# Optimization experiments

Measured on AMD Instinct MI355X. Metric: run time of the kernel, lower is better.

## Reference

```python
import jax, jax.numpy as jnp
import numpy as np

B, T1, T2, NFEAT, H = 8, 512, 1500, 1024, 16
DK = NFEAT // H


def setup_inputs() -> dict:
    key = jax.random.key(0)
    ks = jax.random.split(key, 8)
    s = 0.02
    return {
        "x": jax.random.normal(ks[0], (B, T1, NFEAT), dtype=jnp.float32),
        "memory": jax.random.normal(ks[1], (B, T2, NFEAT), dtype=jnp.float32),
        "memory_mask": jnp.ones((B, 1, T2), dtype=jnp.int32),
        "Wq": jax.random.normal(ks[2], (NFEAT, NFEAT), dtype=jnp.float32) * s,
        "bq": jnp.zeros((NFEAT,), dtype=jnp.float32),
        "Wkv": jax.random.normal(ks[3], (NFEAT, 2 * NFEAT), dtype=jnp.float32) * s,
        "bkv": jnp.zeros((2 * NFEAT,), dtype=jnp.float32),
        "Wout": jax.random.normal(ks[4], (NFEAT, NFEAT), dtype=jnp.float32) * s,
        "bout": jnp.zeros((NFEAT,), dtype=jnp.float32),
    }


def reference(x, memory, memory_mask, Wq, bq, Wkv, bkv, Wout, bout):
    b, t1, _ = x.shape
    t2 = memory.shape[1]
    # projections (W stored as (in, out))
    q = x @ Wq + bq                                   # (b, t1, n_feat)
    kv = memory @ Wkv + bkv                           # (b, t2, 2*n_feat)
    k, v = jnp.split(kv, 2, axis=-1)
    q_h = q.reshape(b, t1, H, DK).transpose(0, 2, 1, 3)   # (b,h,t1,dk)
    k_h = k.reshape(b, t2, H, DK).transpose(0, 2, 1, 3)   # (b,h,t2,dk)
    v_h = v.reshape(b, t2, H, DK).transpose(0, 2, 1, 3)   # (b,h,t2,dk)
    q_h = q_h * (DK ** -0.5)
    scores = jnp.einsum("bhqd,bhkd->bhqk", q_h, k_h)      # (b,h,t1,t2)
    mask0 = (memory_mask[:, None, :, :] == 0)             # (b,1,1 or t1,t2)
    scores = jnp.where(mask0, -jnp.inf, scores)
    attn = jax.nn.softmax(scores, axis=-1)
    attn = jnp.where(mask0, 0.0, attn)
    ctx = jnp.einsum("bhqk,bhkd->bhqd", attn, v_h)        # (b,h,t1,dk)
    ctx = ctx.transpose(0, 2, 1, 3).reshape(b, t1, H * DK)
    return ctx @ Wout + bout
```

## Files before the change

### kernel.cpp

```cpp
#include <hip/hip_runtime.h>
#include <cstdint>
#include <cstddef>

typedef __attribute__((ext_vector_type(8))) short short8;
typedef __attribute__((ext_vector_type(4))) float f32x4;

typedef __attribute__((address_space(3))) unsigned int lds_u32;
typedef const __attribute__((address_space(1))) unsigned int glb_u32;

__device__ __forceinline__ void gl_lds16(const void* g, void* l) {
  __builtin_amdgcn_global_load_lds((glb_u32*)g, (lds_u32*)l, 16, 0, 0);
}

__device__ __forceinline__ unsigned short bf16_rne(float f) {
  unsigned int u = __float_as_uint(f);
  u += 0x7FFFu + ((u >> 16) & 1u);
  return (unsigned short)(u >> 16);
}

__device__ __forceinline__ void cvt_body(const float* __restrict__ in,
                                         unsigned short* __restrict__ out,
                                         int i, int n8) {
  if (i >= n8) return;
  float4 a = reinterpret_cast<const float4*>(in)[2 * i];
  float4 b = reinterpret_cast<const float4*>(in)[2 * i + 1];
  short8 v;
  v[0] = (short)bf16_rne(a.x); v[1] = (short)bf16_rne(a.y);
  v[2] = (short)bf16_rne(a.z); v[3] = (short)bf16_rne(a.w);
  v[4] = (short)bf16_rne(b.x); v[5] = (short)bf16_rne(b.y);
  v[6] = (short)bf16_rne(b.z); v[7] = (short)bf16_rne(b.w);
  reinterpret_cast<short8*>(out)[i] = v;
}

__global__ void __launch_bounds__(256) k_prep(const float* __restrict__ x,
                                              const float* __restrict__ mem,
                                              const float* __restrict__ Wq,
                                              const float* __restrict__ Wkv,
                                              const float* __restrict__ Wout,
                                              unsigned short* __restrict__ xb,
                                              unsigned short* __restrict__ mb,
                                              unsigned short* __restrict__ wqT,
                                              unsigned short* __restrict__ wkvT,
                                              unsigned short* __restrict__ woutT,
                                              unsigned short* __restrict__ pk,
                                              unsigned short* __restrict__ pv) {
  __shared__ float t[64][65];
  const int bid = blockIdx.x, tid = threadIdx.x;
  if (bid < 2048) {
    cvt_body(x, xb, bid * 256 + tid, 524288);
  } else if (bid < 8048) {
    cvt_body(mem, mb, (bid - 2048) * 256 + tid, 1536000);
  } else if (bid < 9072) {
    const float* W; unsigned short* WT; int R = 1024, C; int bid2, bx, by;
    if (bid < 8304)      { W = Wq;   WT = wqT;   C = 1024; bid2 = bid - 8048; bx = bid2 & 15; by = bid2 >> 4; }
    else if (bid < 8816) { W = Wkv;  WT = wkvT;  C = 2048; bid2 = bid - 8304; bx = bid2 & 31; by = bid2 >> 5; }
    else                 { W = Wout; WT = woutT; C = 1024; bid2 = bid - 8816; bx = bid2 & 15; by = bid2 >> 4; }
    const int c0 = bx * 64, r0 = by * 64;
    const int lr = tid >> 6, lc = tid & 63;
#pragma unroll
    for (int i = 0; i < 16; ++i)
      t[i * 4 + lr][lc] = W[(size_t)(r0 + i * 4 + lr) * C + c0 + lc];
    __syncthreads();
#pragma unroll
    for (int i = 0; i < 16; ++i) {
      int ro = i * 4 + lr;
      WT[(size_t)(c0 + ro) * R + r0 + lc] = bf16_rne(t[lc][ro]);
    }
  } else {
    int i = (bid - 9072) * 256 + tid;
    if (i >= 128 * 36 * 64) return;
    int head = i / (36 * 64);
    int rem = i - head * (36 * 64);
    int t2 = rem / 64 + 1500;
    int dk = rem & 63;
    size_t ik = ((size_t)(head * 24 + 23) * 8 + (dk >> 3)) * 512 + (t2 & 63) * 8 + (dk & 7);
    size_t iv = ((size_t)(head * 24 + 23) * 8 + ((t2 >> 3) & 7)) * 512 + dk * 8 + (t2 & 7);
    pk[ik] = 0;
    pv[iv] = 0;
  }
}

template <int MODE>
__global__ void __launch_bounds__(256) k_gemm(const unsigned short* __restrict__ A,
                                              const unsigned short* __restrict__ BT,
                                              const float* __restrict__ bias,
                                              void* __restrict__ out1,
                                              void* __restrict__ out2,
                                              int M, int K) {
  __shared__ unsigned short As[128 * 64];
  __shared__ unsigned short Bs[128 * 64];
  const int tid = threadIdx.x;
  const int lane = tid & 63;
  const int wid = tid >> 6;
  const int grp = lane >> 4, lm = lane & 15;

  constexpr int NBY = (MODE == 1) ? 16 : 8;
  constexpr int NWG = (MODE == 1) ? 94 * 16 : 32 * 8;
  constexpr int CPX = NWG / 8;
  const int bid = blockIdx.x;
  const int logical = (bid & 7) * CPX + (bid >> 3);
  const int m0 = (logical / NBY) * 128, n0 = (logical % NBY) * 128;

  const int wm = (wid >> 1) * 64, wn = (wid & 1) * 64;
  const int srow = tid >> 3;
  const int sx = ((tid & 7) * 16) ^ ((srow & 7) << 4);

  f32x4 acc[4][4] = {};

  const int nkt = K >> 6;
  for (int kt = 0; kt < nkt; ++kt) {
    __syncthreads();
#pragma unroll
    for (int c = 0; c < 4; ++c) {
      int row = c * 32 + srow;
      int ra = m0 + row; if (ra > M - 1) ra = M - 1;
      gl_lds16(A + (size_t)ra * K + kt * 64 + (sx >> 1), As + c * 2048 + tid * 8);
      gl_lds16(BT + (size_t)(n0 + row) * K + kt * 64 + (sx >> 1), Bs + c * 2048 + tid * 8);
    }
    __syncthreads();

    short8 af[4][2], bfr[4][2];
#pragma unroll
    for (int m = 0; m < 4; ++m)
#pragma unroll
      for (int ks = 0; ks < 2; ++ks) {
        int row = wm + m * 16 + lm;
        int off = (ks * 64 + grp * 16) ^ ((row & 7) << 4);
        af[m][ks] = *reinterpret_cast<const short8*>(&As[row * 64 + (off >> 1)]);
      }
#pragma unroll
    for (int n = 0; n < 4; ++n)
#pragma unroll
      for (int ks = 0; ks < 2; ++ks) {
        int row = wn + n * 16 + lm;
        int off = (ks * 64 + grp * 16) ^ ((row & 7) << 4);
        bfr[n][ks] = *reinterpret_cast<const short8*>(&Bs[row * 64 + (off >> 1)]);
      }
#pragma unroll
    for (int m = 0; m < 4; ++m)
#pragma unroll
      for (int n = 0; n < 4; ++n)
#pragma unroll
        for (int ks = 0; ks < 2; ++ks)
          acc[m][n] = __builtin_amdgcn_mfma_f32_16x16x32_bf16(af[m][ks], bfr[n][ks],
                                                              acc[m][n], 0, 0, 0);
  }

#pragma unroll
  for (int m = 0; m < 4; ++m) {
    int rbase = m0 + wm + m * 16 + grp * 4;
#pragma unroll
    for (int n = 0; n < 4; ++n) {
      int cg = n0 + wn + n * 16 + lm;
      float bs = bias[cg];
#pragma unroll
      for (int r = 0; r < 4; ++r) {
        int row = rbase + r;
        float v = acc[m][n][r] + bs;
        if (MODE == 0) {
          v *= 0.180336884f;
          int b = row >> 9, t1 = row & 511, h = cg >> 6, dk = cg & 63;
          ((unsigned short*)out1)[(((size_t)b * 16 + h) * 512 + t1) * 64 + dk] = bf16_rne(v);
        } else if (MODE == 1) {
          if (row < M) {
            int b = row / 1500, t2 = row - b * 1500;
            if (cg < 1024) {
              int h = cg >> 6, dk = cg & 63;
              int head = b * 16 + h;
              size_t idx = ((size_t)(head * 24 + (t2 >> 6)) * 8 + (dk >> 3)) * 512 +
                           (t2 & 63) * 8 + (dk & 7);
              ((unsigned short*)out1)[idx] = bf16_rne(v);
            } else {
              int h = (cg - 1024) >> 6, dk = (cg - 1024) & 63;
              int head = b * 16 + h;
              size_t idx = ((size_t)(head * 24 + (t2 >> 6)) * 8 + ((t2 >> 3) & 7)) * 512 +
                           dk * 8 + (t2 & 7);
              ((unsigned short*)out2)[idx] = bf16_rne(v);
            }
          }
        } else {
          ((float*)out1)[(size_t)row * 1024 + cg] = v;
        }
      }
    }
  }
}

__global__ void __launch_bounds__(256) k_attn(const unsigned short* __restrict__ Q,
                                              const unsigned short* __restrict__ PK,
                                              const unsigned short* __restrict__ PV,
                                              const int* __restrict__ mask,
                                              float* __restrict__ po,
                                              float* __restrict__ dn) {
  __shared__ unsigned short Ps[4][16 * 64];
  const int tid = threadIdx.x, lane = tid & 63, wid = tid >> 6;
  const int grp = lane >> 4, lm = lane & 15;
  const int bid = blockIdx.x;
  const int logical = (bid & 7) * 256 + (bid >> 3);
  const int head = logical >> 4, qt = (logical >> 1) & 7, half = logical & 1;
  const int b = head >> 4, h = head & 15;
  const int kt0 = half * 12;

  const unsigned short* qbase = Q + ((size_t)head * 512 + qt * 64) * 64;
  const unsigned short* kf = PK + (size_t)head * 98304 + grp * 512 + lm * 8;
  const unsigned short* vf = PV + (size_t)head * 98304 + grp * 512 + lm * 8;
  const int* mrow = mask + b * 1500;

  short8 aq[2];
#pragma unroll
  for (int ks = 0; ks < 2; ++ks)
    aq[ks] = *reinterpret_cast<const short8*>(qbase + (wid * 16 + lm) * 64 + ks * 32 + grp * 8);

  unsigned long long mlo = 0ull;
#pragma unroll
  for (int i = 0; i < 48; ++i) {
    int col = (kt0 + (i >> 2)) * 64 + (i & 3) * 16 + lm;
    unsigned int ok = (col < 1500) ? (mrow[col] != 0 ? 1u : 0u) : 0u;
    mlo |= (unsigned long long)ok << i;
  }

  f32x4 O[4] = {};
  f32x4 O4 = {0.f, 0.f, 0.f, 0.f};
  const short8 onesb = {(short)0x3F80, (short)0x3F80, (short)0x3F80, (short)0x3F80,
                        (short)0x3F80, (short)0x3F80, (short)0x3F80, (short)0x3F80};

  short8 bk[4][2];
#pragma unroll
  for (int n = 0; n < 4; ++n)
#pragma unroll
    for (int ks = 0; ks < 2; ++ks)
      bk[n][ks] = *reinterpret_cast<const short8*>(kf + (size_t)kt0 * 4096 + ks * 2048 + n * 128);

  for (int kt = kt0; kt < kt0 + 12; ++kt) {
    short8 bv[4][2];
#pragma unroll
    for (int n2 = 0; n2 < 4; ++n2)
#pragma unroll
      for (int ks = 0; ks < 2; ++ks)
        bv[n2][ks] = *reinterpret_cast<const short8*>(vf + (size_t)kt * 4096 + ks * 2048 + n2 * 128);

    f32x4 s[4];
#pragma unroll
    for (int n = 0; n < 4; ++n) {
      s[n] = f32x4{0.f, 0.f, 0.f, 0.f};
#pragma unroll
      for (int ks = 0; ks < 2; ++ks)
        s[n] = __builtin_amdgcn_mfma_f32_16x16x32_bf16(aq[ks], bk[n][ks], s[n], 0, 0, 0);
    }

    if (kt < kt0 + 11) {
#pragma unroll
      for (int n = 0; n < 4; ++n)
#pragma unroll
        for (int ks = 0; ks < 2; ++ks)
          bk[n][ks] = *reinterpret_cast<const short8*>(
              kf + (size_t)(kt + 1) * 4096 + ks * 2048 + n * 128);
    }

    unsigned int nib = (unsigned int)mlo & 15u;
    mlo >>= 4;
    float mb4[4];
#pragma unroll
    for (int n = 0; n < 4; ++n) mb4[n] = (nib >> n) & 1u ? -8.0f : -3.0e38f;
#pragma unroll
    for (int n = 0; n < 4; ++n)
#pragma unroll
      for (int r = 0; r < 4; ++r) s[n][r] = exp2f(s[n][r] + mb4[n]);

#pragma unroll
    for (int n = 0; n < 4; ++n)
#pragma unroll
      for (int r = 0; r < 4; ++r) {
        int prow = grp * 4 + r;
        int pb = (n * 16 + lm) * 2;
        Ps[wid][prow * 64 + ((pb ^ ((prow & 7) << 4)) >> 1)] = bf16_rne(s[n][r]);
      }
    short8 pa[2];
#pragma unroll
    for (int ks = 0; ks < 2; ++ks) {
      int off = (ks * 64 + grp * 16) ^ ((lm & 7) << 4);
      pa[ks] = *reinterpret_cast<const short8*>(&Ps[wid][lm * 64 + (off >> 1)]);
    }

#pragma unroll
    for (int n2 = 0; n2 < 4; ++n2)
#pragma unroll
      for (int ks = 0; ks < 2; ++ks)
        O[n2] = __builtin_amdgcn_mfma_f32_16x16x32_bf16(pa[ks], bv[n2][ks], O[n2], 0, 0, 0);
#pragma unroll
    for (int ks = 0; ks < 2; ++ks)
      O4 = __builtin_amdgcn_mfma_f32_16x16x32_bf16(pa[ks], onesb, O4, 0, 0, 0);
  }

  float* orow = po + (size_t)half * 4194304 +
                ((size_t)(b * 512 + qt * 64 + wid * 16 + grp * 4)) * 1024 + h * 64;
#pragma unroll
  for (int r = 0; r < 4; ++r)
#pragma unroll
    for (int n2 = 0; n2 < 4; ++n2)
      orow[r * 1024 + n2 * 16 + lm] = O[n2][r];
  if (lm == 0) {
    int t1g = b * 512 + qt * 64 + wid * 16 + grp * 4;
#pragma unroll
    for (int r = 0; r < 4; ++r)
      dn[half * 65536 + (t1g + r) * 16 + h] = O4[r];
  }
}

__global__ void __launch_bounds__(256) k_comb(const float* __restrict__ po,
                                              const float* __restrict__ dn,
                                              unsigned short* __restrict__ ctx) {
  int idx = blockIdx.x * 256 + threadIdx.x;
  if (idx >= 524288) return;
  int row = idx >> 7, c8 = idx & 127;
  int col0 = c8 * 8, h = c8 >> 3;
  float d = dn[row * 16 + h] + dn[65536 + row * 16 + h];
  float inv = 1.0f / d;
  const float4* p0 = reinterpret_cast<const float4*>(po + (size_t)row * 1024 + col0);
  const float4* p1 = reinterpret_cast<const float4*>(po + 4194304 + (size_t)row * 1024 + col0);
  float4 a0 = p0[0], a1 = p0[1], b0 = p1[0], b1 = p1[1];
  short8 v;
  v[0] = (short)bf16_rne((a0.x + b0.x) * inv);
  v[1] = (short)bf16_rne((a0.y + b0.y) * inv);
  v[2] = (short)bf16_rne((a0.z + b0.z) * inv);
  v[3] = (short)bf16_rne((a0.w + b0.w) * inv);
  v[4] = (short)bf16_rne((a1.x + b1.x) * inv);
  v[5] = (short)bf16_rne((a1.y + b1.y) * inv);
  v[6] = (short)bf16_rne((a1.z + b1.z) * inv);
  v[7] = (short)bf16_rne((a1.w + b1.w) * inv);
  reinterpret_cast<short8*>(ctx)[idx] = v;
}

extern "C" void kernel_launch(void* const* d_in, const int* in_sizes, int n_in,
                              void* d_out, int out_size, void* d_ws, size_t ws_size,
                              hipStream_t stream) {
  const float* x = (const float*)d_in[0];
  const float* mem = (const float*)d_in[1];
  const int* mask = (const int*)d_in[2];
  const float* Wq = (const float*)d_in[3];
  const float* bq = (const float*)d_in[4];
  const float* Wkv = (const float*)d_in[5];
  const float* bkv = (const float*)d_in[6];
  const float* Wout = (const float*)d_in[7];
  const float* bout = (const float*)d_in[8];

  uint8_t* w = (uint8_t*)d_ws;
  unsigned short* xb    = (unsigned short*)(w);
  unsigned short* mb    = (unsigned short*)(w + 8388608);
  unsigned short* wqT   = (unsigned short*)(w + 32964608);
  unsigned short* wkvT  = (unsigned short*)(w + 35061760);
  unsigned short* woutT = (unsigned short*)(w + 39256064);
  unsigned short* qb    = (unsigned short*)(w + 41353216);
  unsigned short* kb    = (unsigned short*)(w + 49741824);
  unsigned short* vtb   = (unsigned short*)(w + 74907648);
  unsigned short* ctx   = (unsigned short*)(w + 100073472);
  float* po             = (float*)(w);
  float* dn             = (float*)(w + 33554432);

  k_prep<<<10224, 256, 0, stream>>>(x, mem, Wq, Wkv, Wout, xb, mb, wqT, wkvT, woutT, kb, vtb);
  k_gemm<0><<<256, 256, 0, stream>>>(xb, wqT, bq, qb, nullptr, 4096, 1024);
  k_gemm<1><<<1504, 256, 0, stream>>>(mb, wkvT, bkv, kb, vtb, 12000, 1024);
  k_attn<<<2048, 256, 0, stream>>>(qb, kb, vtb, mask, po, dn);
  k_comb<<<2048, 256, 0, stream>>>(po, dn, ctx);
  k_gemm<2><<<256, 256, 0, stream>>>(ctx, woutT, bout, d_out, nullptr, 4096, 1024);
}
```

Before: 222.3 us.

## Triple-buffer GEMM LDS loads and widen tiles to 128x256 with 512 threads

Reworks the projection GEMM kernel to use a three-stage LDS ring buffer, issuing global-to-LDS loads two k-tiles ahead and using vmcnt waits instead of a sync before and after every tile. Tiles grow to 128x256 with 8 waves per block, halving the grid sizes. The goal is to overlap memory loads with MFMA work and to reuse each A tile across more of N. In exchange, LDS per block rises to 144 KB, which caps occupancy at one block per CU, and the GEMM grids drop to 128 and 752 blocks, which may underfill the GPU. NKT is hardcoded to 16, which assumes K=1024.

```diff
diff --git a/kernel.cpp b/kernel.cpp
--- a/kernel.cpp
+++ b/kernel.cpp
@@ -81,43 +81,63 @@
 }
 
 template <int MODE>
-__global__ void __launch_bounds__(256) k_gemm(const unsigned short* __restrict__ A,
+__global__ void __launch_bounds__(512) k_gemm(const unsigned short* __restrict__ A,
                                               const unsigned short* __restrict__ BT,
                                               const float* __restrict__ bias,
                                               void* __restrict__ out1,
                                               void* __restrict__ out2,
                                               int M, int K) {
-  __shared__ unsigned short As[128 * 64];
-  __shared__ unsigned short Bs[128 * 64];
+  __shared__ unsigned short As[3][128 * 64];
+  __shared__ unsigned short Bs[3][256 * 64];
   const int tid = threadIdx.x;
   const int lane = tid & 63;
   const int wid = tid >> 6;
   const int grp = lane >> 4, lm = lane & 15;
 
-  constexpr int NBY = (MODE == 1) ? 16 : 8;
-  constexpr int NWG = (MODE == 1) ? 94 * 16 : 32 * 8;
+  constexpr int NBY = (MODE == 1) ? 8 : 4;
+  constexpr int NWG = (MODE == 1) ? 94 * 8 : 32 * 4;
   constexpr int CPX = NWG / 8;
   const int bid = blockIdx.x;
   const int logical = (bid & 7) * CPX + (bid >> 3);
-  const int m0 = (logical / NBY) * 128, n0 = (logical % NBY) * 128;
-
-  const int wm = (wid >> 1) * 64, wn = (wid & 1) * 64;
+  const int m0 = (logical / NBY) * 128, n0 = (logical % NBY) * 256;
+
+  const int wm = (wid >> 2) * 64, wn = (wid & 3) * 64;
   const int srow = tid >> 3;
-  const int sx = ((tid & 7) * 16) ^ ((srow & 7) << 4);
+  const int scolb = (tid & 7) * 16;
+
+  constexpr int NKT = 16;
+
+#define STAGE(kt, buf)                                                        \
+  {                                                                           \
+    _Pragma("unroll") for (int j = 0; j < 2; ++j) {                           \
+      int row = j * 64 + srow;                                                \
+      int sxb = scolb ^ ((row & 7) << 4);                                     \
+      int ra = m0 + row; if (ra > M - 1) ra = M - 1;                          \
+      gl_lds16(A + (size_t)ra * K + (kt) * 64 + (sxb >> 1),                   \
+               &As[buf][0] + j * 4096 + tid * 8);                             \
+    }                                                                         \
+    _Pragma("unroll") for (int j = 0; j < 4; ++j) {                           \
+      int row = j * 64 + srow;                                                \
+      int sxb = scolb ^ ((row & 7) << 4);                                     \
+      gl_lds16(BT + (size_t)(n0 + row) * K + (kt) * 64 + (sxb >> 1),          \
+               &Bs[buf][0] + j * 4096 + tid * 8);                             \
+    }                                                                         \
+  }
 
   f32x4 acc[4][4] = {};
 
-  const int nkt = K >> 6;
-  for (int kt = 0; kt < nkt; ++kt) {
-    __syncthreads();
-#pragma unroll
-    for (int c = 0; c < 4; ++c) {
-      int row = c * 32 + srow;
-      int ra = m0 + row; if (ra > M - 1) ra = M - 1;
-      gl_lds16(A + (size_t)ra * K + kt * 64 + (sx >> 1), As + c * 2048 + tid * 8);
-      gl_lds16(BT + (size_t)(n0 + row) * K + kt * 64 + (sx >> 1), Bs + c * 2048 + tid * 8);
-    }
-    __syncthreads();
+  STAGE(0, 0);
+  STAGE(1, 1);
+  asm volatile("s_waitcnt vmcnt(6)" ::: "memory");
+  __builtin_amdgcn_s_barrier();
+  __builtin_amdgcn_sched_barrier(0);
+
+  for (int t = 0; t < NKT; ++t) {
+    const int cb = t % 3;
+    if (t + 2 < NKT) {
+      const int nb = (t + 2) % 3;
+      if (nb == 0) STAGE(t + 2, 0) else if (nb == 1) STAGE(t + 2, 1) else STAGE(t + 2, 2);
+    }
 
     short8 af[4][2], bfr[4][2];
 #pragma unroll
@@ -126,7 +146,7 @@
       for (int ks = 0; ks < 2; ++ks) {
         int row = wm + m * 16 + lm;
         int off = (ks * 64 + grp * 16) ^ ((row & 7) << 4);
-        af[m][ks] = *reinterpret_cast<const short8*>(&As[row * 64 + (off >> 1)]);
+        af[m][ks] = *reinterpret_cast<const short8*>(&As[cb][row * 64 + (off >> 1)]);
       }
 #pragma unroll
     for (int n = 0; n < 4; ++n)
@@ -134,7 +154,7 @@
       for (int ks = 0; ks < 2; ++ks) {
         int row = wn + n * 16 + lm;
         int off = (ks * 64 + grp * 16) ^ ((row & 7) << 4);
-        bfr[n][ks] = *reinterpret_cast<const short8*>(&Bs[row * 64 + (off >> 1)]);
+        bfr[n][ks] = *reinterpret_cast<const short8*>(&Bs[cb][row * 64 + (off >> 1)]);
       }
 #pragma unroll
     for (int m = 0; m < 4; ++m)
@@ -144,7 +164,13 @@
         for (int ks = 0; ks < 2; ++ks)
           acc[m][n] = __builtin_amdgcn_mfma_f32_16x16x32_bf16(af[m][ks], bfr[n][ks],
                                                               acc[m][n], 0, 0, 0);
-  }
+
+    if (t < NKT - 2) asm volatile("s_waitcnt vmcnt(6)" ::: "memory");
+    else             asm volatile("s_waitcnt vmcnt(0)" ::: "memory");
+    __builtin_amdgcn_s_barrier();
+    __builtin_amdgcn_sched_barrier(0);
+  }
+#undef STAGE
 
 #pragma unroll
   for (int m = 0; m < 4; ++m) {
@@ -358,9 +384,9 @@
   float* dn             = (float*)(w + 33554432);
 
   k_prep<<<10224, 256, 0, stream>>>(x, mem, Wq, Wkv, Wout, xb, mb, wqT, wkvT, woutT, kb, vtb);
-  k_gemm<0><<<256, 256, 0, stream>>>(xb, wqT, bq, qb, nullptr, 4096, 1024);
-  k_gemm<1><<<1504, 256, 0, stream>>>(mb, wkvT, bkv, kb, vtb, 12000, 1024);
+  k_gemm<0><<<128, 512, 0, stream>>>(xb, wqT, bq, qb, nullptr, 4096, 1024);
+  k_gemm<1><<<752, 512, 0, stream>>>(mb, wkvT, bkv, kb, vtb, 12000, 1024);
   k_attn<<<2048, 256, 0, stream>>>(qb, kb, vtb, mask, po, dn);
   k_comb<<<2048, 256, 0, stream>>>(po, dn, ctx);
-  k_gemm<2><<<256, 256, 0, stream>>>(ctx, woutT, bout, d_out, nullptr, 4096, 1024);
-}
+  k_gemm<2><<<128, 512, 0, stream>>>(ctx, woutT, bout, d_out, nullptr, 4096, 1024);
+}
```

After: 236.8 us. +6.5%, slower.
